# Kernel tuning notes

Measured on AMD Instinct MI355X. Metric: run time of the kernel, lower is better.

Reference implementation:

```python
import jax, jax.numpy as jnp
import numpy as np

B, H, W, C = 4, 64, 64, 256
CQ = C // 8


def setup_inputs() -> dict:
    key = jax.random.key(0)
    ks = jax.random.split(key, 5)
    scale = 0.02
    inputs = jax.random.normal(ks[0], (B, H, W, C), dtype=jnp.float32)
    wq = jax.random.normal(ks[1], (C, CQ), dtype=jnp.float32) * scale
    bq = jnp.zeros((CQ,), dtype=jnp.float32)
    wk = jax.random.normal(ks[2], (C, CQ), dtype=jnp.float32) * scale
    bk = jnp.zeros((CQ,), dtype=jnp.float32)
    wv = jax.random.normal(ks[3], (C, C), dtype=jnp.float32) * scale
    bv = jnp.zeros((C,), dtype=jnp.float32)
    gamma = jax.random.normal(ks[4], (), dtype=jnp.float32)
    return {"inputs": inputs, "wq": wq, "bq": bq, "wk": wk, "bk": bk,
            "wv": wv, "bv": bv, "gamma": gamma}


def reference(inputs, wq, bq, wk, bk, wv, bv, gamma):
    b, h, w, c = inputs.shape
    n = h * w
    x = inputs.reshape(b, n, c)  # [B, N, C]
    # 1x1 convs == per-pixel linear projections
    q = x @ wq + bq              # [B, N, Cq]
    k = x @ wk + bk              # [B, N, Cq]
    v = x @ wv + bv              # [B, N, C]
    # energy = Q K^T (no sqrt scaling, as in the original)
    energy = jnp.einsum('bnd,bmd->bnm', q, k)      # [B, N, N]
    attention = jax.nn.softmax(energy, axis=-1)    # softmax over keys
    # x_out = V^T @ attention^T -> per query: sum_m attn[n,m] * v[m]
    x_out = jnp.einsum('bnm,bmc->bnc', attention, v)  # [B, N, C]
    x_out = x_out.reshape(b, h, w, c)
    return gamma * x_out + inputs
```

## Files before the change

kernel.cpp:

```cpp
#include <hip/hip_runtime.h>
#include <hip/hip_bf16.h>

typedef __attribute__((ext_vector_type(8))) short bf16x8;
typedef __attribute__((ext_vector_type(4))) float f32x4;
typedef __attribute__((ext_vector_type(16))) float f32x16;
typedef __attribute__((ext_vector_type(4))) int int4v;

#define NB 4
#define NN 4096
#define NC 256
#define NSPLIT 4
#define KEYS_PER_SPLIT 1024
#define KT_ITERS 16

__device__ __forceinline__ unsigned short f2bf(float f) {
    unsigned u = __builtin_bit_cast(unsigned, f);
    u += 0x7fffu + ((u >> 16) & 1u);
    return (unsigned short)(u >> 16);
}
__device__ __forceinline__ float bf2f(unsigned short u) {
    unsigned v = ((unsigned)u) << 16;
    return __builtin_bit_cast(float, v);
}
__device__ __forceinline__ void load_lds16(const void* g, void* l) {
    __builtin_amdgcn_global_load_lds(
        (const __attribute__((address_space(1))) void*)g,
        (__attribute__((address_space(3))) void*)l, 16, 0, 0);
}
__device__ __forceinline__ unsigned cvtpk(float lo, float hi) {
    unsigned d;
    asm("v_cvt_pk_bf16_f32 %0, %1, %2" : "=v"(d) : "v"(lo), "v"(hi));
    return d;
}
__device__ __forceinline__ void pl32swap(unsigned &a, unsigned &b) {
    asm volatile("v_permlane32_swap_b32 %0, %1" : "+v"(a), "+v"(b));
}

__global__ __launch_bounds__(256) void wt_kernel(
    const float* __restrict__ wq, const float* __restrict__ wk,
    const float* __restrict__ wv, unsigned short* __restrict__ wt)
{
    const int c = blockIdx.x;
    const int k = threadIdx.x;
    float v;
    if (c < 32)      v = wq[k * 32 + c];
    else if (c < 64) v = wk[k * 32 + (c - 32)];
    else             v = wv[k * 256 + (c - 64)];
    wt[c * 256 + k] = f2bf(v);
}

__global__ __launch_bounds__(256) void proj_kernel(
    const float* __restrict__ x,
    const unsigned short* __restrict__ wt,
    const float* __restrict__ bq, const float* __restrict__ bk,
    const float* __restrict__ bv,
    unsigned short* __restrict__ q_ws,
    unsigned short* __restrict__ k_ws,
    unsigned short* __restrict__ vt_ws)
{
    const int lane = threadIdx.x & 63;
    const int w    = threadIdx.x >> 6;
    const int l15  = lane & 15, hh = lane >> 4;
    const int m0   = blockIdx.x * 16;
    const int ct0  = w * 5;

    f32x4 acc[5];
    #pragma unroll
    for (int i = 0; i < 5; ++i) acc[i] = f32x4{0.f, 0.f, 0.f, 0.f};

    const float* xrow = x + (size_t)(m0 + l15) * 256 + hh * 8;
    #pragma unroll
    for (int ks = 0; ks < 8; ++ks) {
        float4 xa = ((const float4*)(xrow + ks * 32))[0];
        float4 xb = ((const float4*)(xrow + ks * 32))[1];
        bf16x8 afrag;
        afrag[0] = (short)f2bf(xa.x); afrag[1] = (short)f2bf(xa.y);
        afrag[2] = (short)f2bf(xa.z); afrag[3] = (short)f2bf(xa.w);
        afrag[4] = (short)f2bf(xb.x); afrag[5] = (short)f2bf(xb.y);
        afrag[6] = (short)f2bf(xb.z); afrag[7] = (short)f2bf(xb.w);
        #pragma unroll
        for (int c = 0; c < 5; ++c) {
            bf16x8 bfrag = *(const bf16x8*)(wt + (size_t)((ct0 + c) * 16 + l15) * 256 + ks * 32 + hh * 8);
            acc[c] = __builtin_amdgcn_mfma_f32_16x16x32_bf16(afrag, bfrag, acc[c], 0, 0, 0);
        }
    }

    const int b    = m0 >> 12;
    const int nloc = m0 & 4095;
    #pragma unroll
    for (int c = 0; c < 5; ++c) {
        const int ct = ct0 + c;
        const int c0 = ct * 16;
        float bias;
        if (c0 < 32)      bias = bq[c0 + l15];
        else if (c0 < 64) bias = bk[c0 - 32 + l15];
        else              bias = bv[c0 - 64 + l15];
        if (c0 < 64) {
            unsigned short* dst = (c0 < 32) ? q_ws : k_ws;
            const int cc = (c0 < 32) ? c0 : (c0 - 32);
            #pragma unroll
            for (int i = 0; i < 4; ++i)
                dst[(size_t)(m0 + hh * 4 + i) * 32 + cc + l15] = f2bf(acc[c][i] + bias);
        } else {
            const int cc = c0 - 64 + l15;
            #pragma unroll
            for (int i = 0; i < 4; i += 2) {
                unsigned lo = f2bf(acc[c][i]     + bias);
                unsigned hi = f2bf(acc[c][i + 1] + bias);
                *(unsigned*)(vt_ws + ((size_t)b * 256 + cc) * 4096 + nloc + hh * 4 + i)
                    = lo | (hi << 16);
            }
        }
    }
}

__global__ __launch_bounds__(512, 4) void attn_kernel(
    const unsigned short* __restrict__ q_ws,
    const unsigned short* __restrict__ k_ws,
    const unsigned short* __restrict__ vt_ws,
    unsigned short* __restrict__ opart,
    float* __restrict__ lpart)
{
    __shared__ unsigned short vt_lds[256 * 64];

    const int lane = threadIdx.x & 63;
    const int wid  = threadIdx.x >> 6;
    const int l31  = lane & 31;
    const int hi   = lane >> 5;
    const int wr   = wid >> 1;
    const int wc   = wid & 1;

    const int xcd   = blockIdx.x & 7;
    const int j     = blockIdx.x >> 3;
    const int combo = xcd * 2 + (j >> 5);
    const int qtile = j & 31;
    const int split = combo >> 2;
    const int b     = combo & 3;
    const int q0    = qtile * 128;
    const int key0  = split * KEYS_PER_SPLIT;

    bf16x8 aq[2];
    #pragma unroll
    for (int cs = 0; cs < 2; ++cs)
        aq[cs] = *(const bf16x8*)(q_ws +
            (size_t)(b * 4096 + q0 + wr * 32 + l31) * 32 + cs * 16 + hi * 8);

    f32x16 acc[4];
    #pragma unroll
    for (int ct = 0; ct < 4; ++ct)
        #pragma unroll
        for (int r = 0; r < 16; ++r) acc[ct][r] = 0.f;
    float lsum = 0.f;

    const unsigned short* vt_base = vt_ws + (size_t)b * 256 * 4096;
    const unsigned short* k_base  = k_ws + (size_t)b * 4096 * 32;

    for (int kt = 0; kt < KT_ITERS; ++kt) {
        const int kb = key0 + kt * 64;
        __syncthreads();

        #pragma unroll
        for (int e = 0; e < 4; ++e) {
            int idx  = e * 512 + threadIdx.x;
            int c    = idx >> 3;
            int slot = idx & 7;
            const unsigned short* src = vt_base + (size_t)c * 4096 + kb + ((slot ^ (c & 7)) << 3);
            load_lds16(src, (char*)vt_lds + idx * 16);
        }

        unsigned pa[4][4];
        #pragma unroll
        for (int ktile = 0; ktile < 2; ++ktile) {
            bf16x8 ak0 = *(const bf16x8*)(k_base +
                (size_t)(kb + ktile * 32 + l31) * 32 + hi * 8);
            bf16x8 ak1 = *(const bf16x8*)(k_base +
                (size_t)(kb + ktile * 32 + l31) * 32 + 16 + hi * 8);
            f32x16 e0;
            #pragma unroll
            for (int r = 0; r < 16; ++r) e0[r] = 0.f;
            e0 = __builtin_amdgcn_mfma_f32_32x32x16_bf16(ak0, aq[0], e0, 0, 0, 0);
            e0 = __builtin_amdgcn_mfma_f32_32x32x16_bf16(ak1, aq[1], e0, 0, 0, 0);

            float s = 0.f;
            #pragma unroll
            for (int h = 0; h < 2; ++h) {
                float p0 = __expf(e0[h*8+0]), p1 = __expf(e0[h*8+1]);
                float p2 = __expf(e0[h*8+2]), p3 = __expf(e0[h*8+3]);
                float p4 = __expf(e0[h*8+4]), p5 = __expf(e0[h*8+5]);
                float p6 = __expf(e0[h*8+6]), p7 = __expf(e0[h*8+7]);
                s += ((p0 + p1) + (p2 + p3)) + ((p4 + p5) + (p6 + p7));
                unsigned d0 = cvtpk(p0, p1);
                unsigned d1 = cvtpk(p2, p3);
                unsigned d2 = cvtpk(p4, p5);
                unsigned d3 = cvtpk(p6, p7);
                pl32swap(d0, d2);
                pl32swap(d1, d3);
                const int ks = ktile * 2 + h;
                pa[ks][0] = d0; pa[ks][1] = d1;
                pa[ks][2] = d2; pa[ks][3] = d3;
            }
            lsum += s;
        }
        __syncthreads();

        __builtin_amdgcn_s_setprio(1);
        #pragma unroll
        for (int ks = 0; ks < 4; ++ks) {
            union { unsigned u[4]; bf16x8 v; } cvt;
            cvt.u[0] = pa[ks][0]; cvt.u[1] = pa[ks][1];
            cvt.u[2] = pa[ks][2]; cvt.u[3] = pa[ks][3];
            #pragma unroll
            for (int ct = 0; ct < 4; ++ct) {
                int c = wc * 128 + ct * 32 + l31;
                int chunk = ks * 2 + hi;
                bf16x8 bvf = *(const bf16x8*)((char*)vt_lds + c * 128 + ((chunk ^ (c & 7)) << 4));
                acc[ct] = __builtin_amdgcn_mfma_f32_32x32x16_bf16(cvt.v, bvf, acc[ct], 0, 0, 0);
            }
        }
        __builtin_amdgcn_s_setprio(0);
    }

    lsum += __shfl_xor(lsum, 32);

    const size_t rowb = (size_t)(split * 4 + b) * 4096 + q0 + wr * 32;
    if (wc == 0 && hi == 0)
        lpart[rowb + l31] = lsum;

    #pragma unroll
    for (int ct = 0; ct < 4; ++ct) {
        int col = wc * 128 + ct * 32 + l31;
        #pragma unroll
        for (int rr = 0; rr < 16; ++rr) {
            int row = (rr & 3) + 8 * (rr >> 2) + 4 * hi;
            opart[(rowb + row) * 256 + col] = f2bf(acc[ct][rr]);
        }
    }
}

__global__ __launch_bounds__(256) void combine_kernel(
    const unsigned short* __restrict__ opart,
    const float* __restrict__ lpart,
    const float* __restrict__ x,
    const float* __restrict__ gamma_p,
    float* __restrict__ out)
{
    const int t  = blockIdx.x * 256 + threadIdx.x;
    const int r  = t >> 5;
    const int c0 = (t & 31) * 8;
    const float gamma = gamma_p[0];

    float sumO[8];
    #pragma unroll
    for (int j = 0; j < 8; ++j) sumO[j] = 0.f;
    float suml = 0.f;
    #pragma unroll
    for (int s = 0; s < NSPLIT; ++s) {
        bf16x8 o = *(const bf16x8*)(opart + ((size_t)(s * 16384 + r)) * 256 + c0);
        #pragma unroll
        for (int j = 0; j < 8; ++j) sumO[j] += bf2f((unsigned short)o[j]);
        suml += lpart[s * 16384 + r];
    }
    const float inv = gamma / suml;
    const size_t base = (size_t)r * 256 + c0;
    float4 x0 = *(const float4*)(x + base);
    float4 x1 = *(const float4*)(x + base + 4);
    float4 o0, o1;
    o0.x = sumO[0] * inv + x0.x; o0.y = sumO[1] * inv + x0.y;
    o0.z = sumO[2] * inv + x0.z; o0.w = sumO[3] * inv + x0.w;
    o1.x = sumO[4] * inv + x1.x; o1.y = sumO[5] * inv + x1.y;
    o1.z = sumO[6] * inv + x1.z; o1.w = sumO[7] * inv + x1.w;
    *(float4*)(out + base)     = o0;
    *(float4*)(out + base + 4) = o1;
}

extern "C" void kernel_launch(void* const* d_in, const int* in_sizes, int n_in,
                              void* d_out, int out_size, void* d_ws, size_t ws_size,
                              hipStream_t stream) {
    const float* x     = (const float*)d_in[0];
    const float* wq    = (const float*)d_in[1];
    const float* bq    = (const float*)d_in[2];
    const float* wk    = (const float*)d_in[3];
    const float* bk    = (const float*)d_in[4];
    const float* wv    = (const float*)d_in[5];
    const float* bv    = (const float*)d_in[6];
    const float* gamma = (const float*)d_in[7];
    float* out = (float*)d_out;

    char* ws = (char*)d_ws;
    unsigned short* wt    = (unsigned short*)(ws);
    unsigned short* q_ws  = (unsigned short*)(ws + 163840);
    unsigned short* k_ws  = (unsigned short*)(ws + 1212416);
    unsigned short* vt_ws = (unsigned short*)(ws + 2260992);
    unsigned short* opart = (unsigned short*)(ws + 10649600);
    float*          lpart = (float*)(ws + 44204032);

    wt_kernel     <<<320,  256, 0, stream>>>(wq, wk, wv, wt);
    proj_kernel   <<<1024, 256, 0, stream>>>(x, wt, bq, bk, bv, q_ws, k_ws, vt_ws);
    attn_kernel   <<<512,  512, 0, stream>>>(q_ws, k_ws, vt_ws, opart, lpart);
    combine_kernel<<<2048, 256, 0, stream>>>(opart, lpart, x, gamma, out);
}
```

Measured before the change: 104.8 us.

## Double-buffer V tiles in LDS and fold log2e into K for exp2

Splits the V-tile LDS buffer into two halves. The next key tile's V is prefetched with global_load_lds while the current tile's QK^T, exp and PV MFMAs run, synchronised by raw s_barrier plus an explicit vmcnt wait. Separately, it scales the K weights and bias by log2(e) at projection time so the softmax numerator can use the native v_exp_f32 (exp2) and skip a multiply per element. The cost is double the LDS per block, which can limit how many blocks fit on a CU, and the hand-written wait count relies on in-order completion of vector memory loads.

```diff
diff --git a/kernel.cpp b/kernel.cpp
--- a/kernel.cpp
+++ b/kernel.cpp
@@ -12,6 +12,7 @@
 #define NSPLIT 4
 #define KEYS_PER_SPLIT 1024
 #define KT_ITERS 16
+#define LOG2E 1.4426950408889634f
 
 __device__ __forceinline__ unsigned short f2bf(float f) {
     unsigned u = __builtin_bit_cast(unsigned, f);
@@ -34,6 +35,11 @@
 }
 __device__ __forceinline__ void pl32swap(unsigned &a, unsigned &b) {
     asm volatile("v_permlane32_swap_b32 %0, %1" : "+v"(a), "+v"(b));
+}
+__device__ __forceinline__ float fexp2(float x) {
+    float r;
+    asm("v_exp_f32 %0, %1" : "=v"(r) : "v"(x));
+    return r;
 }
 
 __global__ __launch_bounds__(256) void wt_kernel(
@@ -44,7 +50,7 @@
     const int k = threadIdx.x;
     float v;
     if (c < 32)      v = wq[k * 32 + c];
-    else if (c < 64) v = wk[k * 32 + (c - 32)];
+    else if (c < 64) v = wk[k * 32 + (c - 32)] * LOG2E;
     else             v = wv[k * 256 + (c - 64)];
     wt[c * 256 + k] = f2bf(v);
 }
@@ -93,7 +99,7 @@
         const int c0 = ct * 16;
         float bias;
         if (c0 < 32)      bias = bq[c0 + l15];
-        else if (c0 < 64) bias = bk[c0 - 32 + l15];
+        else if (c0 < 64) bias = bk[c0 - 32 + l15] * LOG2E;
         else              bias = bv[c0 - 64 + l15];
         if (c0 < 64) {
             unsigned short* dst = (c0 < 32) ? q_ws : k_ws;
@@ -121,7 +127,7 @@
     unsigned short* __restrict__ opart,
     float* __restrict__ lpart)
 {
-    __shared__ unsigned short vt_lds[256 * 64];
+    __shared__ unsigned short vt_lds[2 * 256 * 64];
 
     const int lane = threadIdx.x & 63;
     const int wid  = threadIdx.x >> 6;
@@ -155,10 +161,8 @@
     const unsigned short* vt_base = vt_ws + (size_t)b * 256 * 4096;
     const unsigned short* k_base  = k_ws + (size_t)b * 4096 * 32;
 
-    for (int kt = 0; kt < KT_ITERS; ++kt) {
-        const int kb = key0 + kt * 64;
-        __syncthreads();
-
+    {
+        const int kb = key0;
         #pragma unroll
         for (int e = 0; e < 4; ++e) {
             int idx  = e * 512 + threadIdx.x;
@@ -167,27 +171,54 @@
             const unsigned short* src = vt_base + (size_t)c * 4096 + kb + ((slot ^ (c & 7)) << 3);
             load_lds16(src, (char*)vt_lds + idx * 16);
         }
+    }
+
+    for (int kt = 0; kt < KT_ITERS; ++kt) {
+        const int kb = key0 + kt * 64;
+        unsigned short* vbuf = vt_lds + (kt & 1) * (256 * 64);
+
+        __builtin_amdgcn_sched_barrier(0);
+        __builtin_amdgcn_s_barrier();
+        __builtin_amdgcn_sched_barrier(0);
+
+        bf16x8 ak[2][2];
+        #pragma unroll
+        for (int ktile = 0; ktile < 2; ++ktile) {
+            ak[ktile][0] = *(const bf16x8*)(k_base + (size_t)(kb + ktile * 32 + l31) * 32 + hi * 8);
+            ak[ktile][1] = *(const bf16x8*)(k_base + (size_t)(kb + ktile * 32 + l31) * 32 + 16 + hi * 8);
+        }
+        __builtin_amdgcn_sched_barrier(0);
+
+        if (kt + 1 < KT_ITERS) {
+            unsigned short* nbuf = vt_lds + ((kt + 1) & 1) * (256 * 64);
+            const int nkb = key0 + (kt + 1) * 64;
+            #pragma unroll
+            for (int e = 0; e < 4; ++e) {
+                int idx  = e * 512 + threadIdx.x;
+                int c    = idx >> 3;
+                int slot = idx & 7;
+                const unsigned short* src = vt_base + (size_t)c * 4096 + nkb + ((slot ^ (c & 7)) << 3);
+                load_lds16(src, (char*)nbuf + idx * 16);
+            }
+        }
+        __builtin_amdgcn_sched_barrier(0);
 
         unsigned pa[4][4];
         #pragma unroll
         for (int ktile = 0; ktile < 2; ++ktile) {
-            bf16x8 ak0 = *(const bf16x8*)(k_base +
-                (size_t)(kb + ktile * 32 + l31) * 32 + hi * 8);
-            bf16x8 ak1 = *(const bf16x8*)(k_base +
-                (size_t)(kb + ktile * 32 + l31) * 32 + 16 + hi * 8);
             f32x16 e0;
             #pragma unroll
             for (int r = 0; r < 16; ++r) e0[r] = 0.f;
-            e0 = __builtin_amdgcn_mfma_f32_32x32x16_bf16(ak0, aq[0], e0, 0, 0, 0);
-            e0 = __builtin_amdgcn_mfma_f32_32x32x16_bf16(ak1, aq[1], e0, 0, 0, 0);
+            e0 = __builtin_amdgcn_mfma_f32_32x32x16_bf16(ak[ktile][0], aq[0], e0, 0, 0, 0);
+            e0 = __builtin_amdgcn_mfma_f32_32x32x16_bf16(ak[ktile][1], aq[1], e0, 0, 0, 0);
 
             float s = 0.f;
             #pragma unroll
             for (int h = 0; h < 2; ++h) {
-                float p0 = __expf(e0[h*8+0]), p1 = __expf(e0[h*8+1]);
-                float p2 = __expf(e0[h*8+2]), p3 = __expf(e0[h*8+3]);
-                float p4 = __expf(e0[h*8+4]), p5 = __expf(e0[h*8+5]);
-                float p6 = __expf(e0[h*8+6]), p7 = __expf(e0[h*8+7]);
+                float p0 = fexp2(e0[h*8+0]), p1 = fexp2(e0[h*8+1]);
+                float p2 = fexp2(e0[h*8+2]), p3 = fexp2(e0[h*8+3]);
+                float p4 = fexp2(e0[h*8+4]), p5 = fexp2(e0[h*8+5]);
+                float p6 = fexp2(e0[h*8+6]), p7 = fexp2(e0[h*8+7]);
                 s += ((p0 + p1) + (p2 + p3)) + ((p4 + p5) + (p6 + p7));
                 unsigned d0 = cvtpk(p0, p1);
                 unsigned d1 = cvtpk(p2, p3);
@@ -201,7 +232,11 @@
             }
             lsum += s;
         }
-        __syncthreads();
+
+        asm volatile("s_waitcnt vmcnt(4)" ::: "memory");
+        __builtin_amdgcn_sched_barrier(0);
+        __builtin_amdgcn_s_barrier();
+        __builtin_amdgcn_sched_barrier(0);
 
         __builtin_amdgcn_s_setprio(1);
         #pragma unroll
@@ -213,7 +248,7 @@
             for (int ct = 0; ct < 4; ++ct) {
                 int c = wc * 128 + ct * 32 + l31;
                 int chunk = ks * 2 + hi;
-                bf16x8 bvf = *(const bf16x8*)((char*)vt_lds + c * 128 + ((chunk ^ (c & 7)) << 4));
+                bf16x8 bvf = *(const bf16x8*)((char*)vbuf + c * 128 + ((chunk ^ (c & 7)) << 4));
                 acc[ct] = __builtin_amdgcn_mfma_f32_32x32x16_bf16(cvt.v, bvf, acc[ct], 0, 0, 0);
             }
         }
```

After: 106.6 us. About the same (+1.6%).
